# Kernel optimization log

Hardware: AMD Instinct MI355X
Metric: run time of the kernel (lower is better)

Reference implementation:

```python
import jax, jax.numpy as jnp
import numpy as np

E = 400000   # total edges
G = 64       # num graphs
H = 256      # hidden_dim
NN = 20000   # node id range
FRONTIER_BONUS = 0.5


def layer_norm(x, g, b, eps=1e-5):
    m = jnp.mean(x, axis=-1, keepdims=True)
    v = jnp.var(x, axis=-1, keepdims=True)
    return (x - m) / jnp.sqrt(v + eps) * g + b


def setup_inputs() -> dict:
    key = jax.random.key(0)
    ks = jax.random.split(key, 20)
    s = 0.02
    inp = {
        "edge_tokens": jax.random.normal(ks[0], (E, H), jnp.float32),
        "question_tokens": jax.random.normal(ks[1], (G, H), jnp.float32),
        "edge_batch": jnp.sort(jax.random.randint(ks[2], (E,), 0, G)),
        "selected_mask": jax.random.bernoulli(ks[3], 0.3, (E,)),
        "edge_heads": jax.random.randint(ks[4], (E,), 0, NN),
        "edge_tails": jax.random.randint(ks[5], (E,), 0, NN),
        "current_tail": jax.random.randint(ks[6], (G,), 0, NN),
        # edge_proj params: LayerNorm(H+2) -> Linear(H+2,H) -> GELU -> Linear(H,H) -> GELU
        "ln1_g": jnp.ones((H + 2,), jnp.float32),
        "ln1_b": jnp.zeros((H + 2,), jnp.float32),
        "W1": s * jax.random.normal(ks[7], (H + 2, H), jnp.float32),
        "b1": jnp.zeros((H,), jnp.float32),
        "W2": s * jax.random.normal(ks[8], (H, H), jnp.float32),
        "b2": jnp.zeros((H,), jnp.float32),
        # selection_head: Linear(H,1)
        "sel_w": s * jax.random.normal(ks[9], (H, 1), jnp.float32),
        "sel_b": jnp.zeros((1,), jnp.float32),
        # stop_head: LayerNorm(2H) -> Linear(2H,H) -> GELU -> Linear(H,1)
        "ln2_g": jnp.ones((2 * H,), jnp.float32),
        "ln2_b": jnp.zeros((2 * H,), jnp.float32),
        "sW1": s * jax.random.normal(ks[10], (2 * H, H), jnp.float32),
        "sb1": jnp.zeros((H,), jnp.float32),
        "sW2": s * jax.random.normal(ks[11], (H, 1), jnp.float32),
        "sb2": jnp.zeros((1,), jnp.float32),
    }
    return inp


def reference(edge_tokens, question_tokens, edge_batch, selected_mask,
              edge_heads, edge_tails, current_tail,
              ln1_g, ln1_b, W1, b1, W2, b2, sel_w, sel_b,
              ln2_g, ln2_b, sW1, sb1, sW2, sb2):
    num_graphs = question_tokens.shape[0]
    candidate = ~selected_mask
    cur_e = current_tail[edge_batch]                       # [E] gather by graph id
    frontier = candidate & ((edge_heads == cur_e) | (edge_tails == cur_e))
    aux = jnp.stack([candidate.astype(jnp.float32), frontier.astype(jnp.float32)], axis=-1)
    x = jnp.concatenate([edge_tokens, aux], axis=-1)       # [E, H+2]
    h = layer_norm(x, ln1_g, ln1_b)
    h = jax.nn.gelu(h @ W1 + b1, approximate=False)        # Dropout is identity in eval
    h = jax.nn.gelu(h @ W2 + b2, approximate=False)        # edge_repr [E, H]
    edge_logits = (h @ sel_w)[:, 0] + sel_b[0]
    edge_logits = edge_logits + FRONTIER_BONUS * frontier.astype(jnp.float32)
    counts = jax.ops.segment_sum(jnp.ones((h.shape[0],), jnp.float32), edge_batch, num_segments=num_graphs)
    counts = jnp.clip(counts, 1.0)                          # bincount.clamp(min=1)
    pooled = jax.ops.segment_sum(h, edge_batch, num_segments=num_graphs) / counts[:, None]
    s_in = jnp.concatenate([pooled, question_tokens], axis=-1)  # [G, 2H]
    s = layer_norm(s_in, ln2_g, ln2_b)
    s = jax.nn.gelu(s @ sW1 + sb1, approximate=False)
    stop_logits = (s @ sW2)[:, 0] + sb2[0]
    return edge_logits, stop_logits, pooled
```

## Files before the change

### kernel.cpp

```cpp
#include <hip/hip_runtime.h>
#include <hip/hip_bf16.h>
#include <cstdint>


typedef __bf16 bf16x8 __attribute__((ext_vector_type(8)));
typedef float  f32x4  __attribute__((ext_vector_type(4)));

typedef __attribute__((address_space(1))) const char gas_char;
typedef __attribute__((address_space(3))) char las_char;

__device__ __forceinline__ float gelu_f(float x) {
  float x2 = x * x;
  float t1 = __builtin_fmaf(0.1029444f, x2, 2.3022078f);
  float a  = x * t1;
  float e;
  asm("v_exp_f32 %0, %1" : "=v"(e) : "v"(a));
  float r;
  asm("v_rcp_f32 %0, %1" : "=v"(r) : "v"(e + 1.0f));
  return x - x * r;
}

__global__ void prep_pack(const float* __restrict__ W1, const float* __restrict__ W2,
                          const float* __restrict__ ln1g,
                          __bf16* __restrict__ W1p, __bf16* __restrict__ W2p) {
  int gid = blockIdx.x * blockDim.x + threadIdx.x;
  int m  = gid >> 13;
  int b  = (gid >> 6) & 127;
  int l  = gid & 63;
  int kt = b >> 4, nt = b & 15;
  int k0 = kt * 32 + ((l >> 4) << 3);
  int n  = nt * 16 + (l & 15);
  const float* W = m ? W2 : W1;
  bf16x8 v;
#pragma unroll
  for (int i = 0; i < 8; ++i) {
    int k = k0 + i;
    float wv = W[k * 256 + n];
    if (!m) wv *= ln1g[k];
    v[i] = (__bf16)wv;
  }
  __bf16* dst = m ? W2p : W1p;
  *(bf16x8*)(dst + (size_t)(b * 64 + l) * 8) = v;
}

__global__ void prep_vec(const float* __restrict__ W1, const float* __restrict__ ln1g,
                         const float* __restrict__ ln1b, const float* __restrict__ b1,
                         const unsigned* __restrict__ smask_words,
                         float* __restrict__ C0, float* __restrict__ GW6,
                         float* __restrict__ GW7, int* __restrict__ maskIsByte) {
  __shared__ float red[4][256];
  const int n = threadIdx.x & 255, c = threadIdx.x >> 8;
  const int k0 = c * 64, k1 = (c == 3) ? 258 : k0 + 64;
  float s = 0.f;
#pragma unroll 4
  for (int k = k0; k < k1; ++k) s += ln1b[k] * W1[k * 256 + n];
  red[c][n] = s;
  __syncthreads();
  if (c == 0) {
    C0[n]  = b1[n] + red[0][n] + red[1][n] + red[2][n] + red[3][n];
    GW6[n] = ln1g[256] * W1[256 * 256 + n];
    GW7[n] = ln1g[257] * W1[257 * 256 + n];
  }
  if (threadIdx.x == 0) {
    int big = 0;
    for (int i = 0; i < 64; ++i) { if (smask_words[i] > 1u) big = 1; }
    *maskIsByte = big;
  }
}

#define EPB 64

__device__ __forceinline__ void stage4(const char* gsrc, char* ldst) {
  __builtin_amdgcn_global_load_lds((gas_char*)gsrc, (las_char*)ldst, 16, 0, 0);
  __builtin_amdgcn_global_load_lds((gas_char*)(gsrc + 1024), (las_char*)(ldst + 1024), 16, 0, 0);
  __builtin_amdgcn_global_load_lds((gas_char*)(gsrc + 2048), (las_char*)(ldst + 2048), 16, 0, 0);
  __builtin_amdgcn_global_load_lds((gas_char*)(gsrc + 3072), (las_char*)(ldst + 3072), 16, 0, 0);
}

__device__ __forceinline__ void gemm8(const char* __restrict__ Wp, const char* nextWp,
                                      char* B0, char* B1,
                                      const char* aBase, unsigned swA, unsigned gA,
                                      int bOff, int woff, int l16, f32x4 (&acc)[4][4]) {
#pragma unroll
  for (int kt = 0; kt < 8; ++kt) {
    if (kt == 0) asm volatile("s_waitcnt vmcnt(4)" ::: "memory");
    else         asm volatile("s_waitcnt vmcnt(0)" ::: "memory");
    __builtin_amdgcn_s_barrier();
    if (kt >= 1 && kt < 7)
      stage4(Wp + (kt + 1) * 16384 + woff + l16, ((kt & 1) ? B0 : B1) + woff);
    if (kt == 7 && nextWp)
      stage4(nextWp + woff + l16, B0 + woff);
    const char* bb = (kt & 1) ? B1 : B0;
    bf16x8 av[4], bv[4];
#pragma unroll
    for (int rf = 0; rf < 4; ++rf)
      av[rf] = *(const bf16x8*)(aBase + rf * 8192 + (((unsigned)(kt * 64) + gA) ^ swA));
#pragma unroll
    for (int cf = 0; cf < 4; ++cf)
      bv[cf] = *(const bf16x8*)(bb + bOff + (cf << 10));
#pragma unroll
    for (int rf = 0; rf < 4; ++rf)
#pragma unroll
      for (int cf = 0; cf < 4; ++cf)
        acc[rf][cf] = __builtin_amdgcn_mfma_f32_16x16x32_bf16(av[rf], bv[cf], acc[rf][cf], 0, 0, 0);
  }
  __builtin_amdgcn_s_barrier();
}

__global__ __launch_bounds__(256, 2) void edge_kernel(
    const float* __restrict__ tok, const int* __restrict__ ebatch,
    const unsigned char* __restrict__ smaskB,
    const int* __restrict__ eheads, const int* __restrict__ etails,
    const int* __restrict__ curtail,
    const __bf16* __restrict__ W1p, const __bf16* __restrict__ W2p,
    const float* __restrict__ C0v, const float* __restrict__ GW6v,
    const float* __restrict__ GW7v, const float* __restrict__ b2v,
    const float* __restrict__ selwv, const float* __restrict__ selbv,
    const int* __restrict__ maskFlag,
    float* __restrict__ outLogits, float* __restrict__ pooledAcc,
    float* __restrict__ cnts) {
  __shared__ __align__(16) char As_[64 * 512];
  __shared__ __align__(16) char Bs_[2][16384];
  __shared__ float sZa0[64], sZa1[64], sFront[64];
  __shared__ float sLog[64][4];
  __shared__ int sG[64];

  const int t = threadIdx.x;
  const int w = t >> 6, l = t & 63;
  const int base = blockIdx.x * EPB;
  const int l16 = l << 4;
  const int woff = __builtin_amdgcn_readfirstlane(w << 12);

  const char* W1c = (const char*)W1p;
  const char* W2c = (const char*)W2p;

  stage4(W1c + woff + l16, Bs_[0] + woff);
  stage4(W1c + 16384 + woff + l16, Bs_[1] + woff);

  if (t < 64) {
    int ge = base + t;
    int g  = ebatch[ge];
    int mb = *maskFlag;
    int mv = mb ? (int)smaskB[ge] : ((const int*)smaskB)[ge];
    int cand = (mv == 0);
    int cur  = curtail[g];
    int fr   = cand && ((eheads[ge] == cur) || (etails[ge] == cur));
    sZa0[t] = (float)cand; sZa1[t] = (float)fr; sFront[t] = (float)fr; sG[t] = g;
  }
  __syncthreads();

  if (t == 0) {
    int cg = sG[0]; float run = 1.f;
    for (int e = 1; e < EPB; ++e) {
      int g = sG[e];
      if (g == cg) run += 1.f;
      else { atomicAdd(&cnts[cg], run); cg = g; run = 1.f; }
    }
    atomicAdd(&cnts[cg], run);
  }

  {
    const int e = t >> 2, q = t & 3;
    const float* rp = tok + (size_t)(base + e) * 256 + q * 4;
    float4 v[16];
    float s = 0.f, s2 = 0.f;
#pragma unroll
    for (int j = 0; j < 16; ++j) {
      v[j] = *(const float4*)(rp + j * 16);
      s  += v[j].x + v[j].y + v[j].z + v[j].w;
      s2 += v[j].x * v[j].x + v[j].y * v[j].y + v[j].z * v[j].z + v[j].w * v[j].w;
    }
    float a0 = 0.f, a1 = 0.f;
    if (q == 0) { a0 = sZa0[e]; a1 = sZa1[e]; s += a0 + a1; s2 += a0 + a1; }
    s  += __shfl_xor(s, 1);  s  += __shfl_xor(s, 2);
    s2 += __shfl_xor(s2, 1); s2 += __shfl_xor(s2, 2);
    const float mean = s * (1.0f / 258.0f);
    const float var  = s2 * (1.0f / 258.0f) - mean * mean;
    const float rstd = rsqrtf(var + 1e-5f);
    const unsigned sw = (unsigned)(e & 7) << 4;
#pragma unroll
    for (int j = 0; j < 16; ++j) {
      union { __bf16 h[4]; uint2 u; } cv;
      cv.h[0] = (__bf16)((v[j].x - mean) * rstd);
      cv.h[1] = (__bf16)((v[j].y - mean) * rstd);
      cv.h[2] = (__bf16)((v[j].z - mean) * rstd);
      cv.h[3] = (__bf16)((v[j].w - mean) * rstd);
      unsigned off = (unsigned)(q * 8 + j * 32);
      *(uint2*)(As_ + e * 512 + (off ^ sw)) = cv.u;
    }
    if (q == 0) {
      sZa0[e] = (a0 - mean) * rstd;
      sZa1[e] = (a1 - mean) * rstd;
    }
  }
  __syncthreads();

  const int rA = l & 15;
  const int r0 = (l >> 4) << 2;
  float c0r[4], w6r[4], w7r[4], b2r[4], lwr[4];
  const float selbr = selbv[0];
#pragma unroll
  for (int cf = 0; cf < 4; ++cf) {
    int col = w * 64 + cf * 16 + rA;
    c0r[cf] = C0v[col]; w6r[cf] = GW6v[col]; w7r[cf] = GW7v[col];
    b2r[cf] = b2v[col]; lwr[cf] = selwv[col];
  }
  f32x4 za0q[4], za1q[4];
#pragma unroll
  for (int rf = 0; rf < 4; ++rf) {
    za0q[rf] = *(const f32x4*)&sZa0[rf * 16 + r0];
    za1q[rf] = *(const f32x4*)&sZa1[rf * 16 + r0];
  }
  f32x4 acc[4][4];
#pragma unroll
  for (int rf = 0; rf < 4; ++rf)
#pragma unroll
    for (int cf = 0; cf < 4; ++cf)
#pragma unroll
      for (int i = 0; i < 4; ++i)
        acc[rf][cf][i] = c0r[cf] + za0q[rf][i] * w6r[cf] + za1q[rf][i] * w7r[cf];

  const unsigned swA = (unsigned)(rA & 7) << 4;
  const unsigned gA  = (unsigned)((l >> 4) << 4);
  const char* aBase  = As_ + rA * 512;
  const int bOff     = (w << 12) + l16;

  gemm8(W1c, W2c, Bs_[0], Bs_[1], aBase, swA, gA, bOff, woff, l16, acc);

#pragma unroll
  for (int rf = 0; rf < 4; ++rf)
#pragma unroll
    for (int i = 0; i < 4; ++i) {
      int row = rf * 16 + r0 + i;
      char* rowp = As_ + row * 512;
      unsigned sw = (unsigned)(row & 7) << 4;
#pragma unroll
      for (int cf = 0; cf < 4; ++cf) {
        int col = w * 64 + cf * 16 + rA;
        *(__bf16*)(rowp + (((unsigned)(col * 2)) ^ sw)) = (__bf16)gelu_f(acc[rf][cf][i]);
      }
    }
  stage4(W2c + 16384 + woff + l16, Bs_[1] + woff);
  __syncthreads();

#pragma unroll
  for (int rf = 0; rf < 4; ++rf)
#pragma unroll
    for (int cf = 0; cf < 4; ++cf)
#pragma unroll
      for (int i = 0; i < 4; ++i) acc[rf][cf][i] = b2r[cf];
  gemm8(W2c, nullptr, Bs_[0], Bs_[1], aBase, swA, gA, bOff, woff, l16, acc);

#pragma unroll
  for (int rf = 0; rf < 4; ++rf)
#pragma unroll
    for (int cf = 0; cf < 4; ++cf)
#pragma unroll
      for (int i = 0; i < 4; ++i) acc[rf][cf][i] = gelu_f(acc[rf][cf][i]);

#pragma unroll
  for (int rf = 0; rf < 4; ++rf)
#pragma unroll
    for (int i = 0; i < 4; ++i) {
      float p = acc[rf][0][i] * lwr[0] + acc[rf][1][i] * lwr[1]
              + acc[rf][2][i] * lwr[2] + acc[rf][3][i] * lwr[3];
      p += __shfl_xor(p, 1); p += __shfl_xor(p, 2);
      p += __shfl_xor(p, 4); p += __shfl_xor(p, 8);
      if (rA == 0) sLog[rf * 16 + r0 + i][w] = p;
    }
  __syncthreads();
  if (t < 64)
    outLogits[base + t] = sLog[t][0] + sLog[t][1] + sLog[t][2] + sLog[t][3]
                        + selbr + 0.5f * sFront[t];

  if (sG[0] == sG[EPB - 1]) {
    int g = sG[0];
#pragma unroll
    for (int cf = 0; cf < 4; ++cf) {
      float sv = 0.f;
#pragma unroll
      for (int rf = 0; rf < 4; ++rf)
#pragma unroll
        for (int i = 0; i < 4; ++i) sv += acc[rf][cf][i];
      sv += __shfl_xor(sv, 16);
      sv += __shfl_xor(sv, 32);
      if (l < 16) atomicAdd(&pooledAcc[g * 256 + w * 64 + cf * 16 + l], sv);
    }
  } else {
#pragma unroll
    for (int rf = 0; rf < 4; ++rf)
#pragma unroll
      for (int i = 0; i < 4; ++i) {
        int row = rf * 16 + r0 + i;
        int g = sG[row];
#pragma unroll
        for (int cf = 0; cf < 4; ++cf)
          atomicAdd(&pooledAcc[g * 256 + w * 64 + cf * 16 + rA], acc[rf][cf][i]);
      }
  }
}

__global__ __launch_bounds__(256) void stop_kernel(
    const float* __restrict__ pooledAcc, const float* __restrict__ cnts,
    const float* __restrict__ qtok,
    const float* __restrict__ ln2g, const float* __restrict__ ln2b,
    const float* __restrict__ sW1, const float* __restrict__ sb1,
    const float* __restrict__ sW2, const float* __restrict__ sb2,
    float* __restrict__ outStop, float* __restrict__ outPooled) {
  __shared__ float sIn[512], sLn[512], sRed[8];
  const int t = threadIdx.x, g = blockIdx.x;
  const int w = t >> 6, l = t & 63;
  float c = fmaxf(cnts[g], 1.0f);
  float p = pooledAcc[g * 256 + t] / c;
  outPooled[g * 256 + t] = p;
  sIn[t] = p;
  sIn[256 + t] = qtok[g * 256 + t];
  __syncthreads();
  float a = sIn[t], b = sIn[256 + t];
  float s = a + b, s2 = a * a + b * b;
#pragma unroll
  for (int m = 1; m < 64; m <<= 1) { s += __shfl_xor(s, m); s2 += __shfl_xor(s2, m); }
  if (l == 0) { sRed[w] = s; sRed[4 + w] = s2; }
  __syncthreads();
  s  = sRed[0] + sRed[1] + sRed[2] + sRed[3];
  s2 = sRed[4] + sRed[5] + sRed[6] + sRed[7];
  const float mean = s * (1.0f / 512.0f);
  const float var  = s2 * (1.0f / 512.0f) - mean * mean;
  const float rstd = rsqrtf(var + 1e-5f);
  sLn[t]       = (a - mean) * rstd * ln2g[t] + ln2b[t];
  sLn[256 + t] = (b - mean) * rstd * ln2g[256 + t] + ln2b[256 + t];
  __syncthreads();
  float accv = sb1[t];
#pragma unroll 8
  for (int k = 0; k < 512; ++k) accv += sLn[k] * sW1[k * 256 + t];
  float u = gelu_f(accv);
  float part = u * sW2[t];
#pragma unroll
  for (int m = 1; m < 64; m <<= 1) part += __shfl_xor(part, m);
  if (l == 0) sRed[w] = part;
  __syncthreads();
  if (t == 0) outStop[g] = sRed[0] + sRed[1] + sRed[2] + sRed[3] + sb2[0];
}

extern "C" void kernel_launch(void* const* d_in, const int* in_sizes, int n_in,
                              void* d_out, int out_size, void* d_ws, size_t ws_size,
                              hipStream_t stream) {
  const float* tok   = (const float*)d_in[0];
  const float* qtok  = (const float*)d_in[1];
  const int* ebatch  = (const int*)d_in[2];
  const void* smask  = d_in[3];
  const int* eheads  = (const int*)d_in[4];
  const int* etails  = (const int*)d_in[5];
  const int* curtail = (const int*)d_in[6];
  const float* ln1g  = (const float*)d_in[7];
  const float* ln1b  = (const float*)d_in[8];
  const float* W1    = (const float*)d_in[9];
  const float* b1    = (const float*)d_in[10];
  const float* W2    = (const float*)d_in[11];
  const float* b2    = (const float*)d_in[12];
  const float* selw  = (const float*)d_in[13];
  const float* selb  = (const float*)d_in[14];
  const float* ln2g  = (const float*)d_in[15];
  const float* ln2b  = (const float*)d_in[16];
  const float* sW1   = (const float*)d_in[17];
  const float* sb1   = (const float*)d_in[18];
  const float* sW2   = (const float*)d_in[19];
  const float* sb2   = (const float*)d_in[20];

  const int E = in_sizes[2];
  const int G = in_sizes[1] / 256;

  char* ws = (char*)d_ws;
  __bf16* W1p   = (__bf16*)(ws);
  __bf16* W2p   = (__bf16*)(ws + 131072);
  float*  C0    = (float*)(ws + 262144);
  float*  GW6   = (float*)(ws + 263168);
  float*  GW7   = (float*)(ws + 264192);
  float*  pooled= (float*)(ws + 265216);
  float*  cnts  = (float*)(ws + 330752);
  int*    mflag = (int*)(ws + 331008);
  (void)ws_size; (void)n_in; (void)out_size;

  hipMemsetAsync(ws + 265216, 0, 65536 + 256, stream);

  prep_pack<<<64, 256, 0, stream>>>(W1, W2, ln1g, W1p, W2p);
  prep_vec<<<1, 1024, 0, stream>>>(W1, ln1g, ln1b, b1, (const unsigned*)smask,
                                   C0, GW6, GW7, mflag);
  edge_kernel<<<E / EPB, 256, 0, stream>>>(
      tok, ebatch, (const unsigned char*)smask, eheads, etails, curtail,
      W1p, W2p, C0, GW6, GW7, b2, selw, selb, mflag,
      (float*)d_out, pooled, cnts);
  stop_kernel<<<G, 256, 0, stream>>>(pooled, cnts, qtok, ln2g, ln2b,
                                     sW1, sb1, sW2, sb2,
                                     (float*)d_out + E, (float*)d_out + E + G);
}
```

Before: 350.6 us.

## Make edge kernel persistent with per-wave 32-edge tiles and LDS-resident W1

Replaces the one-block-per-64-edges kernel with a persistent grid of 256 blocks of 512 threads. W1 is loaded once into 128KB of LDS per block, and each wave independently processes 32-edge tiles. The layer norm and the first GEMM keep activations in registers as MFMA B operands, and the hidden layer is redistributed via shuffles, not an LDS round trip. W2 is streamed from global/L2 directly into registers with double buffering. This removes block barriers and repeated weight staging, but adds pressure on registers and on L2 bandwidth for W2, and the 128KB of LDS limits occupancy.

```diff
diff --git a/kernel.cpp b/kernel.cpp
--- a/kernel.cpp
+++ b/kernel.cpp
@@ -18,6 +18,14 @@
   float r;
   asm("v_rcp_f32 %0, %1" : "=v"(r) : "v"(e + 1.0f));
   return x - x * r;
+}
+
+__device__ __forceinline__ bf16x8 as_frag(uint4 u) {
+  union { uint4 u; bf16x8 f; } c; c.u = u; return c.f;
+}
+__device__ __forceinline__ unsigned pk2(float a, float b) {
+  union { __bf16 h[2]; unsigned u; } c;
+  c.h[0] = (__bf16)a; c.h[1] = (__bf16)b; return c.u;
 }
 
 __global__ void prep_pack(const float* __restrict__ W1, const float* __restrict__ W2,
@@ -68,46 +76,7 @@
   }
 }
 
-#define EPB 64
-
-__device__ __forceinline__ void stage4(const char* gsrc, char* ldst) {
-  __builtin_amdgcn_global_load_lds((gas_char*)gsrc, (las_char*)ldst, 16, 0, 0);
-  __builtin_amdgcn_global_load_lds((gas_char*)(gsrc + 1024), (las_char*)(ldst + 1024), 16, 0, 0);
-  __builtin_amdgcn_global_load_lds((gas_char*)(gsrc + 2048), (las_char*)(ldst + 2048), 16, 0, 0);
-  __builtin_amdgcn_global_load_lds((gas_char*)(gsrc + 3072), (las_char*)(ldst + 3072), 16, 0, 0);
-}
-
-__device__ __forceinline__ void gemm8(const char* __restrict__ Wp, const char* nextWp,
-                                      char* B0, char* B1,
-                                      const char* aBase, unsigned swA, unsigned gA,
-                                      int bOff, int woff, int l16, f32x4 (&acc)[4][4]) {
-#pragma unroll
-  for (int kt = 0; kt < 8; ++kt) {
-    if (kt == 0) asm volatile("s_waitcnt vmcnt(4)" ::: "memory");
-    else         asm volatile("s_waitcnt vmcnt(0)" ::: "memory");
-    __builtin_amdgcn_s_barrier();
-    if (kt >= 1 && kt < 7)
-      stage4(Wp + (kt + 1) * 16384 + woff + l16, ((kt & 1) ? B0 : B1) + woff);
-    if (kt == 7 && nextWp)
-      stage4(nextWp + woff + l16, B0 + woff);
-    const char* bb = (kt & 1) ? B1 : B0;
-    bf16x8 av[4], bv[4];
-#pragma unroll
-    for (int rf = 0; rf < 4; ++rf)
-      av[rf] = *(const bf16x8*)(aBase + rf * 8192 + (((unsigned)(kt * 64) + gA) ^ swA));
-#pragma unroll
-    for (int cf = 0; cf < 4; ++cf)
-      bv[cf] = *(const bf16x8*)(bb + bOff + (cf << 10));
-#pragma unroll
-    for (int rf = 0; rf < 4; ++rf)
-#pragma unroll
-      for (int cf = 0; cf < 4; ++cf)
-        acc[rf][cf] = __builtin_amdgcn_mfma_f32_16x16x32_bf16(av[rf], bv[cf], acc[rf][cf], 0, 0, 0);
-  }
-  __builtin_amdgcn_s_barrier();
-}
-
-__global__ __launch_bounds__(256, 2) void edge_kernel(
+__global__ __launch_bounds__(512, 2) void edge_kernel(
     const float* __restrict__ tok, const int* __restrict__ ebatch,
     const unsigned char* __restrict__ smaskB,
     const int* __restrict__ eheads, const int* __restrict__ etails,
@@ -118,184 +87,257 @@
     const float* __restrict__ selwv, const float* __restrict__ selbv,
     const int* __restrict__ maskFlag,
     float* __restrict__ outLogits, float* __restrict__ pooledAcc,
-    float* __restrict__ cnts) {
-  __shared__ __align__(16) char As_[64 * 512];
-  __shared__ __align__(16) char Bs_[2][16384];
-  __shared__ float sZa0[64], sZa1[64], sFront[64];
-  __shared__ float sLog[64][4];
-  __shared__ int sG[64];
-
-  const int t = threadIdx.x;
-  const int w = t >> 6, l = t & 63;
-  const int base = blockIdx.x * EPB;
-  const int l16 = l << 4;
-  const int woff = __builtin_amdgcn_readfirstlane(w << 12);
-
-  const char* W1c = (const char*)W1p;
+    float* __restrict__ cnts, int E) {
+  __shared__ __align__(16) char Wlds[131072];
+  __shared__ float sC0[256], sW6[256], sW7[256], sSelw[256], sB2[256];
+
+  const int t  = threadIdx.x;
+  const int w  = t >> 6, l = t & 63;
+  const int lo = l & 15, g = l >> 4;
+
+  {
+    const char* Wsrc = (const char*)W1p;
+    unsigned woff = __builtin_amdgcn_readfirstlane((unsigned)w * 16384u);
+#pragma unroll
+    for (int it = 0; it < 16; ++it)
+      __builtin_amdgcn_global_load_lds((gas_char*)(Wsrc + woff + it * 1024 + l * 16),
+                                       (las_char*)(Wlds + woff + it * 1024), 16, 0, 0);
+  }
+  if (t < 256) {
+    sC0[t] = C0v[t]; sW6[t] = GW6v[t]; sW7[t] = GW7v[t];
+    sSelw[t] = selwv[t]; sB2[t] = b2v[t];
+  }
+  const int   mb    = *maskFlag;
+  const float selbr = selbv[0];
+  __syncthreads();
+
+  const int totalTiles = E >> 5;
+  const int nWaves = gridDim.x * 8;
   const char* W2c = (const char*)W2p;
 
-  stage4(W1c + woff + l16, Bs_[0] + woff);
-  stage4(W1c + 16384 + woff + l16, Bs_[1] + woff);
-
-  if (t < 64) {
-    int ge = base + t;
-    int g  = ebatch[ge];
-    int mb = *maskFlag;
-    int mv = mb ? (int)smaskB[ge] : ((const int*)smaskB)[ge];
-    int cand = (mv == 0);
-    int cur  = curtail[g];
-    int fr   = cand && ((eheads[ge] == cur) || (etails[ge] == cur));
-    sZa0[t] = (float)cand; sZa1[t] = (float)fr; sFront[t] = (float)fr; sG[t] = g;
-  }
-  __syncthreads();
-
-  if (t == 0) {
-    int cg = sG[0]; float run = 1.f;
-    for (int e = 1; e < EPB; ++e) {
-      int g = sG[e];
-      if (g == cg) run += 1.f;
-      else { atomicAdd(&cnts[cg], run); cg = g; run = 1.f; }
+  for (int tile = blockIdx.x * 8 + w; tile < totalTiles; tile += nWaves) {
+    const int base = tile << 5;
+
+    float candf = 0.f, frontf = 0.f; int gid = 0;
+    if (l < 32) {
+      int ge = base + l;
+      gid = ebatch[ge];
+      int mv = mb ? (int)smaskB[ge] : ((const int*)smaskB)[ge];
+      int cand = (mv == 0);
+      int cur  = curtail[gid];
+      int fr   = cand && ((eheads[ge] == cur) || (etails[ge] == cur));
+      candf = (float)cand; frontf = (float)fr;
     }
-    atomicAdd(&cnts[cg], run);
-  }
-
-  {
-    const int e = t >> 2, q = t & 3;
-    const float* rp = tok + (size_t)(base + e) * 256 + q * 4;
-    float4 v[16];
-    float s = 0.f, s2 = 0.f;
-#pragma unroll
-    for (int j = 0; j < 16; ++j) {
-      v[j] = *(const float4*)(rp + j * 16);
-      s  += v[j].x + v[j].y + v[j].z + v[j].w;
-      s2 += v[j].x * v[j].x + v[j].y * v[j].y + v[j].z * v[j].z + v[j].w * v[j].w;
+    const int g0s = __shfl(gid, 0);
+    const bool uniform =
+        (__ballot((l < 32) ? (gid == g0s) : 1) == ~0ull);
+    {
+      int gp = __shfl(gid, (l == 0) ? 0 : l - 1);
+      bool isb = (l < 32) && (l == 0 || gid != gp);
+      unsigned long long bm = __ballot(isb);
+      if (isb) {
+        unsigned long long m2 = bm >> (l + 1);
+        int run = m2 ? (int)__ffsll((long long)m2) : (32 - l);
+        atomicAdd(&cnts[gid], (float)run);
+      }
     }
-    float a0 = 0.f, a1 = 0.f;
-    if (q == 0) { a0 = sZa0[e]; a1 = sZa1[e]; s += a0 + a1; s2 += a0 + a1; }
-    s  += __shfl_xor(s, 1);  s  += __shfl_xor(s, 2);
-    s2 += __shfl_xor(s2, 1); s2 += __shfl_xor(s2, 2);
-    const float mean = s * (1.0f / 258.0f);
-    const float var  = s2 * (1.0f / 258.0f) - mean * mean;
-    const float rstd = rsqrtf(var + 1e-5f);
-    const unsigned sw = (unsigned)(e & 7) << 4;
-#pragma unroll
-    for (int j = 0; j < 16; ++j) {
-      union { __bf16 h[4]; uint2 u; } cv;
-      cv.h[0] = (__bf16)((v[j].x - mean) * rstd);
-      cv.h[1] = (__bf16)((v[j].y - mean) * rstd);
-      cv.h[2] = (__bf16)((v[j].z - mean) * rstd);
-      cv.h[3] = (__bf16)((v[j].w - mean) * rstd);
-      unsigned off = (unsigned)(q * 8 + j * 32);
-      *(uint2*)(As_ + e * 512 + (off ^ sw)) = cv.u;
+    const float ca = __shfl(candf, lo),      fa = __shfl(frontf, lo);
+    const float cb = __shfl(candf, 16 + lo), fb = __shfl(frontf, 16 + lo);
+
+    uint4 zlnA[8], zlnB[8];
+    float za0a, za1a, za0b, za1b;
+#pragma unroll
+    for (int rr = 0; rr < 2; ++rr) {
+      const int   edge = base + rr * 16 + lo;
+      const float aux0 = rr ? cb : ca, aux1 = rr ? fb : fa;
+      const float* rp = tok + (size_t)edge * 256 + (g << 3);
+      float4 v[16];
+#pragma unroll
+      for (int kt = 0; kt < 8; ++kt) {
+        v[2 * kt]     = *(const float4*)(rp + kt * 32);
+        v[2 * kt + 1] = *(const float4*)(rp + kt * 32 + 4);
+      }
+      float s = 0.f, s2 = 0.f;
+#pragma unroll
+      for (int j = 0; j < 16; ++j) {
+        s  += v[j].x + v[j].y + v[j].z + v[j].w;
+        s2 += v[j].x * v[j].x + v[j].y * v[j].y + v[j].z * v[j].z + v[j].w * v[j].w;
+      }
+      s  += __shfl_xor(s, 16);  s  += __shfl_xor(s, 32);
+      s2 += __shfl_xor(s2, 16); s2 += __shfl_xor(s2, 32);
+      s += aux0 + aux1; s2 += aux0 + aux1;
+      const float mean = s * (1.0f / 258.0f);
+      const float var  = s2 * (1.0f / 258.0f) - mean * mean;
+      const float rstd = rsqrtf(var + 1e-5f);
+      const float nm   = -mean * rstd;
+      uint4* zf = rr ? zlnB : zlnA;
+#pragma unroll
+      for (int kt = 0; kt < 8; ++kt) {
+        union { __bf16 h[8]; uint4 u; } cv;
+#pragma unroll
+        for (int q = 0; q < 4; ++q) {
+          float x0 = (q < 2) ? ((q & 1) ? v[2*kt].z : v[2*kt].x)
+                             : ((q & 1) ? v[2*kt+1].z : v[2*kt+1].x);
+          float x1 = (q < 2) ? ((q & 1) ? v[2*kt].w : v[2*kt].y)
+                             : ((q & 1) ? v[2*kt+1].w : v[2*kt+1].y);
+          cv.h[2*q]   = (__bf16)__builtin_fmaf(x0, rstd, nm);
+          cv.h[2*q+1] = (__bf16)__builtin_fmaf(x1, rstd, nm);
+        }
+        zf[kt] = cv.u;
+      }
+      if (rr) { za0b = __builtin_fmaf(aux0, rstd, nm); za1b = __builtin_fmaf(aux1, rstd, nm); }
+      else    { za0a = __builtin_fmaf(aux0, rstd, nm); za1a = __builtin_fmaf(aux1, rstd, nm); }
     }
-    if (q == 0) {
-      sZa0[e] = (a0 - mean) * rstd;
-      sZa1[e] = (a1 - mean) * rstd;
+
+    uint4 h1f[2][8];
+#pragma unroll
+    for (int half = 0; half < 2; ++half) {
+      f32x4 acc[8][2];
+#pragma unroll
+      for (int jl = 0; jl < 8; ++jl) {
+        const int j = half * 8 + jl;
+        f32x4 c0 = *(const f32x4*)&sC0[j * 16 + g * 4];
+        f32x4 w6 = *(const f32x4*)&sW6[j * 16 + g * 4];
+        f32x4 w7 = *(const f32x4*)&sW7[j * 16 + g * 4];
+#pragma unroll
+        for (int i = 0; i < 4; ++i) {
+          acc[jl][0][i] = c0[i] + za0a * w6[i] + za1a * w7[i];
+          acc[jl][1][i] = c0[i] + za0b * w6[i] + za1b * w7[i];
+        }
+      }
+#pragma unroll
+      for (int kt = 0; kt < 8; ++kt) {
+        bf16x8 afr[8];
+#pragma unroll
+        for (int jl = 0; jl < 8; ++jl)
+          afr[jl] = as_frag(*(const uint4*)(Wlds + (size_t)(kt * 16 + half * 8 + jl) * 1024 + l * 16));
+        bf16x8 bA = as_frag(zlnA[kt]), bB = as_frag(zlnB[kt]);
+#pragma unroll
+        for (int jl = 0; jl < 8; ++jl) {
+          acc[jl][0] = __builtin_amdgcn_mfma_f32_16x16x32_bf16(afr[jl], bA, acc[jl][0], 0, 0, 0);
+          acc[jl][1] = __builtin_amdgcn_mfma_f32_16x16x32_bf16(afr[jl], bB, acc[jl][1], 0, 0, 0);
+        }
+      }
+      unsigned pk[2][8][2];
+#pragma unroll
+      for (int mt = 0; mt < 2; ++mt)
+#pragma unroll
+        for (int jl = 0; jl < 8; ++jl) {
+          pk[mt][jl][0] = pk2(gelu_f(acc[jl][mt][0]), gelu_f(acc[jl][mt][1]));
+          pk[mt][jl][1] = pk2(gelu_f(acc[jl][mt][2]), gelu_f(acc[jl][mt][3]));
+        }
+#pragma unroll
+      for (int mt = 0; mt < 2; ++mt)
+#pragma unroll
+        for (int k2l = 0; k2l < 4; ++k2l) {
+          unsigned dw[4];
+#pragma unroll
+          for (int tt = 0; tt < 4; ++tt) {
+            int src = 16 * (2 * (g & 1) + (tt >> 1)) + lo;
+            unsigned dE = __shfl(pk[mt][2 * k2l][tt & 1], src);
+            unsigned dO = __shfl(pk[mt][2 * k2l + 1][tt & 1], src);
+            dw[tt] = (g >= 2) ? dO : dE;
+          }
+          h1f[mt][half * 4 + k2l] = make_uint4(dw[0], dw[1], dw[2], dw[3]);
+        }
     }
-  }
-  __syncthreads();
-
-  const int rA = l & 15;
-  const int r0 = (l >> 4) << 2;
-  float c0r[4], w6r[4], w7r[4], b2r[4], lwr[4];
-  const float selbr = selbv[0];
-#pragma unroll
-  for (int cf = 0; cf < 4; ++cf) {
-    int col = w * 64 + cf * 16 + rA;
-    c0r[cf] = C0v[col]; w6r[cf] = GW6v[col]; w7r[cf] = GW7v[col];
-    b2r[cf] = b2v[col]; lwr[cf] = selwv[col];
-  }
-  f32x4 za0q[4], za1q[4];
-#pragma unroll
-  for (int rf = 0; rf < 4; ++rf) {
-    za0q[rf] = *(const f32x4*)&sZa0[rf * 16 + r0];
-    za1q[rf] = *(const f32x4*)&sZa1[rf * 16 + r0];
-  }
-  f32x4 acc[4][4];
-#pragma unroll
-  for (int rf = 0; rf < 4; ++rf)
-#pragma unroll
-    for (int cf = 0; cf < 4; ++cf)
-#pragma unroll
-      for (int i = 0; i < 4; ++i)
-        acc[rf][cf][i] = c0r[cf] + za0q[rf][i] * w6r[cf] + za1q[rf][i] * w7r[cf];
-
-  const unsigned swA = (unsigned)(rA & 7) << 4;
-  const unsigned gA  = (unsigned)((l >> 4) << 4);
-  const char* aBase  = As_ + rA * 512;
-  const int bOff     = (w << 12) + l16;
-
-  gemm8(W1c, W2c, Bs_[0], Bs_[1], aBase, swA, gA, bOff, woff, l16, acc);
-
-#pragma unroll
-  for (int rf = 0; rf < 4; ++rf)
-#pragma unroll
-    for (int i = 0; i < 4; ++i) {
-      int row = rf * 16 + r0 + i;
-      char* rowp = As_ + row * 512;
-      unsigned sw = (unsigned)(row & 7) << 4;
-#pragma unroll
-      for (int cf = 0; cf < 4; ++cf) {
-        int col = w * 64 + cf * 16 + rA;
-        *(__bf16*)(rowp + (((unsigned)(col * 2)) ^ sw)) = (__bf16)gelu_f(acc[rf][cf][i]);
+
+    float plog[2][4];
+#pragma unroll
+    for (int mt = 0; mt < 2; ++mt)
+#pragma unroll
+      for (int i = 0; i < 4; ++i) plog[mt][i] = 0.f;
+
+#pragma unroll
+    for (int ch = 0; ch < 2; ++ch) {
+      f32x4 acc2[8][2];
+#pragma unroll
+      for (int c8 = 0; c8 < 8; ++c8) {
+        float bb = sB2[(ch * 8 + c8) * 16 + lo];
+#pragma unroll
+        for (int mt = 0; mt < 2; ++mt)
+#pragma unroll
+          for (int i = 0; i < 4; ++i) acc2[c8][mt][i] = bb;
+      }
+      const char* wbase = W2c + (size_t)ch * 8192 + (size_t)l * 16;
+      uint4 b0[8], b1[8];
+#pragma unroll
+      for (int c8 = 0; c8 < 8; ++c8) b0[c8] = *(const uint4*)(wbase + c8 * 1024);
+#pragma unroll
+      for (int kt2 = 0; kt2 < 8; ++kt2) {
+        if (kt2 < 7) {
+          if (kt2 & 1) {
+#pragma unroll
+            for (int c8 = 0; c8 < 8; ++c8)
+              b0[c8] = *(const uint4*)(wbase + (size_t)(kt2 + 1) * 16384 + c8 * 1024);
+          } else {
+#pragma unroll
+            for (int c8 = 0; c8 < 8; ++c8)
+              b1[c8] = *(const uint4*)(wbase + (size_t)(kt2 + 1) * 16384 + c8 * 1024);
+          }
+        }
+        bf16x8 a0 = as_frag(h1f[0][kt2]), a1 = as_frag(h1f[1][kt2]);
+#pragma unroll
+        for (int c8 = 0; c8 < 8; ++c8) {
+          bf16x8 bf = as_frag((kt2 & 1) ? b1[c8] : b0[c8]);
+          acc2[c8][0] = __builtin_amdgcn_mfma_f32_16x16x32_bf16(a0, bf, acc2[c8][0], 0, 0, 0);
+          acc2[c8][1] = __builtin_amdgcn_mfma_f32_16x16x32_bf16(a1, bf, acc2[c8][1], 0, 0, 0);
+        }
+      }
+#pragma unroll
+      for (int c8 = 0; c8 < 8; ++c8) {
+        float wv = sSelw[(ch * 8 + c8) * 16 + lo];
+#pragma unroll
+        for (int mt = 0; mt < 2; ++mt)
+#pragma unroll
+          for (int i = 0; i < 4; ++i) {
+            acc2[c8][mt][i] = gelu_f(acc2[c8][mt][i]);
+            plog[mt][i] += acc2[c8][mt][i] * wv;
+          }
+      }
+      if (uniform) {
+#pragma unroll
+        for (int c8 = 0; c8 < 8; ++c8) {
+          float pv = 0.f;
+#pragma unroll
+          for (int mt = 0; mt < 2; ++mt)
+#pragma unroll
+            for (int i = 0; i < 4; ++i) pv += acc2[c8][mt][i];
+          pv += __shfl_xor(pv, 16);
+          pv += __shfl_xor(pv, 32);
+          if (l < 16) atomicAdd(&pooledAcc[g0s * 256 + (ch * 8 + c8) * 16 + l], pv);
+        }
+      } else {
+        int gm[2][4];
+#pragma unroll
+        for (int mt = 0; mt < 2; ++mt)
+#pragma unroll
+          for (int i = 0; i < 4; ++i) gm[mt][i] = __shfl(gid, 16 * mt + 4 * g + i);
+#pragma unroll
+        for (int c8 = 0; c8 < 8; ++c8)
+#pragma unroll
+          for (int mt = 0; mt < 2; ++mt)
+#pragma unroll
+            for (int i = 0; i < 4; ++i)
+              atomicAdd(&pooledAcc[gm[mt][i] * 256 + (ch * 8 + c8) * 16 + lo],
+                        acc2[c8][mt][i]);
       }
     }
-  stage4(W2c + 16384 + woff + l16, Bs_[1] + woff);
-  __syncthreads();
-
-#pragma unroll
-  for (int rf = 0; rf < 4; ++rf)
-#pragma unroll
-    for (int cf = 0; cf < 4; ++cf)
-#pragma unroll
-      for (int i = 0; i < 4; ++i) acc[rf][cf][i] = b2r[cf];
-  gemm8(W2c, nullptr, Bs_[0], Bs_[1], aBase, swA, gA, bOff, woff, l16, acc);
-
-#pragma unroll
-  for (int rf = 0; rf < 4; ++rf)
-#pragma unroll
-    for (int cf = 0; cf < 4; ++cf)
-#pragma unroll
-      for (int i = 0; i < 4; ++i) acc[rf][cf][i] = gelu_f(acc[rf][cf][i]);
-
-#pragma unroll
-  for (int rf = 0; rf < 4; ++rf)
-#pragma unroll
-    for (int i = 0; i < 4; ++i) {
-      float p = acc[rf][0][i] * lwr[0] + acc[rf][1][i] * lwr[1]
-              + acc[rf][2][i] * lwr[2] + acc[rf][3][i] * lwr[3];
-      p += __shfl_xor(p, 1); p += __shfl_xor(p, 2);
-      p += __shfl_xor(p, 4); p += __shfl_xor(p, 8);
-      if (rA == 0) sLog[rf * 16 + r0 + i][w] = p;
-    }
-  __syncthreads();
-  if (t < 64)
-    outLogits[base + t] = sLog[t][0] + sLog[t][1] + sLog[t][2] + sLog[t][3]
-                        + selbr + 0.5f * sFront[t];
-
-  if (sG[0] == sG[EPB - 1]) {
-    int g = sG[0];
-#pragma unroll
-    for (int cf = 0; cf < 4; ++cf) {
-      float sv = 0.f;
-#pragma unroll
-      for (int rf = 0; rf < 4; ++rf)
-#pragma unroll
-        for (int i = 0; i < 4; ++i) sv += acc[rf][cf][i];
-      sv += __shfl_xor(sv, 16);
-      sv += __shfl_xor(sv, 32);
-      if (l < 16) atomicAdd(&pooledAcc[g * 256 + w * 64 + cf * 16 + l], sv);
-    }
-  } else {
-#pragma unroll
-    for (int rf = 0; rf < 4; ++rf)
+
+    float fm[2][4];
+#pragma unroll
+    for (int mt = 0; mt < 2; ++mt)
+#pragma unroll
+      for (int i = 0; i < 4; ++i) fm[mt][i] = __shfl(frontf, 16 * mt + 4 * g + i);
+#pragma unroll
+    for (int mt = 0; mt < 2; ++mt)
 #pragma unroll
       for (int i = 0; i < 4; ++i) {
-        int row = rf * 16 + r0 + i;
-        int g = sG[row];
-#pragma unroll
-        for (int cf = 0; cf < 4; ++cf)
-          atomicAdd(&pooledAcc[g * 256 + w * 64 + cf * 16 + rA], acc[rf][cf][i]);
+        float p = plog[mt][i];
+        p += __shfl_xor(p, 1); p += __shfl_xor(p, 2);
+        p += __shfl_xor(p, 4); p += __shfl_xor(p, 8);
+        if (lo == 0)
+          outLogits[base + 16 * mt + 4 * g + i] = p + selbr + 0.5f * fm[mt][i];
       }
   }
 }
@@ -386,10 +428,10 @@
   prep_pack<<<64, 256, 0, stream>>>(W1, W2, ln1g, W1p, W2p);
   prep_vec<<<1, 1024, 0, stream>>>(W1, ln1g, ln1b, b1, (const unsigned*)smask,
                                    C0, GW6, GW7, mflag);
-  edge_kernel<<<E / EPB, 256, 0, stream>>>(
+  edge_kernel<<<256, 512, 0, stream>>>(
       tok, ebatch, (const unsigned char*)smask, eheads, etails, curtail,
       W1p, W2p, C0, GW6, GW7, b2, selw, selb, mflag,
-      (float*)d_out, pooled, cnts);
+      (float*)d_out, pooled, cnts, E);
   stop_kernel<<<G, 256, 0, stream>>>(pooled, cnts, qtok, ln2g, ln2b,
                                      sW1, sb1, sW2, sb2,
                                      (float*)d_out + E, (float*)d_out + E + G);
```

Measured after the change: 826.3 us. 136% more time.

## Load packed weight fragments directly into registers instead of staging through LDS

Applied to the files above, without the earlier changes.

Replaces the LDS double-buffered weight staging (global_load_lds plus barriers per k-tile) with per-wave direct global loads of B fragments into registers, prefetching the next k-tile while the current MFMAs run. This removes the 32KB weight LDS buffer and the per-k-tile barriers. It also drops the occupancy hint of two blocks per CU in the launch bounds and narrows the lifetime of several epilogue constants to ease register pressure. The trade-off is that every wave now reads weights from global/L2 on its own rather than sharing one staged copy, and global load latency sits closer to the MFMA chain.

```diff
diff --git a/kernel.cpp b/kernel.cpp
--- a/kernel.cpp
+++ b/kernel.cpp
@@ -5,9 +5,6 @@
 
 typedef __bf16 bf16x8 __attribute__((ext_vector_type(8)));
 typedef float  f32x4  __attribute__((ext_vector_type(4)));
-
-typedef __attribute__((address_space(1))) const char gas_char;
-typedef __attribute__((address_space(3))) char las_char;
 
 __device__ __forceinline__ float gelu_f(float x) {
   float x2 = x * x;
@@ -18,6 +15,10 @@
   float r;
   asm("v_rcp_f32 %0, %1" : "=v"(r) : "v"(e + 1.0f));
   return x - x * r;
+}
+
+__device__ __forceinline__ bf16x8 as_frag(uint4 u) {
+  union { uint4 u; bf16x8 f; } c; c.u = u; return c.f;
 }
 
 __global__ void prep_pack(const float* __restrict__ W1, const float* __restrict__ W2,
@@ -70,44 +71,37 @@
 
 #define EPB 64
 
-__device__ __forceinline__ void stage4(const char* gsrc, char* ldst) {
-  __builtin_amdgcn_global_load_lds((gas_char*)gsrc, (las_char*)ldst, 16, 0, 0);
-  __builtin_amdgcn_global_load_lds((gas_char*)(gsrc + 1024), (las_char*)(ldst + 1024), 16, 0, 0);
-  __builtin_amdgcn_global_load_lds((gas_char*)(gsrc + 2048), (las_char*)(ldst + 2048), 16, 0, 0);
-  __builtin_amdgcn_global_load_lds((gas_char*)(gsrc + 3072), (las_char*)(ldst + 3072), 16, 0, 0);
-}
-
-__device__ __forceinline__ void gemm8(const char* __restrict__ Wp, const char* nextWp,
-                                      char* B0, char* B1,
-                                      const char* aBase, unsigned swA, unsigned gA,
-                                      int bOff, int woff, int l16, f32x4 (&acc)[4][4]) {
+__device__ __forceinline__ void gemm8_reg(const char* __restrict__ Wp,
+                                          const char* aBase, unsigned swA,
+                                          unsigned gA, int bOff,
+                                          f32x4 (&acc)[4][4]) {
+  uint4 bv[4], bn[4];
+#pragma unroll
+  for (int cf = 0; cf < 4; ++cf)
+    bv[cf] = *(const uint4*)(Wp + bOff + (cf << 10));
 #pragma unroll
   for (int kt = 0; kt < 8; ++kt) {
-    if (kt == 0) asm volatile("s_waitcnt vmcnt(4)" ::: "memory");
-    else         asm volatile("s_waitcnt vmcnt(0)" ::: "memory");
-    __builtin_amdgcn_s_barrier();
-    if (kt >= 1 && kt < 7)
-      stage4(Wp + (kt + 1) * 16384 + woff + l16, ((kt & 1) ? B0 : B1) + woff);
-    if (kt == 7 && nextWp)
-      stage4(nextWp + woff + l16, B0 + woff);
-    const char* bb = (kt & 1) ? B1 : B0;
-    bf16x8 av[4], bv[4];
+    if (kt < 7) {
+#pragma unroll
+      for (int cf = 0; cf < 4; ++cf)
+        bn[cf] = *(const uint4*)(Wp + (kt + 1) * 16384 + bOff + (cf << 10));
+    }
+    bf16x8 av[4];
 #pragma unroll
     for (int rf = 0; rf < 4; ++rf)
       av[rf] = *(const bf16x8*)(aBase + rf * 8192 + (((unsigned)(kt * 64) + gA) ^ swA));
 #pragma unroll
-    for (int cf = 0; cf < 4; ++cf)
-      bv[cf] = *(const bf16x8*)(bb + bOff + (cf << 10));
-#pragma unroll
     for (int rf = 0; rf < 4; ++rf)
 #pragma unroll
       for (int cf = 0; cf < 4; ++cf)
-        acc[rf][cf] = __builtin_amdgcn_mfma_f32_16x16x32_bf16(av[rf], bv[cf], acc[rf][cf], 0, 0, 0);
-  }
-  __builtin_amdgcn_s_barrier();
-}
-
-__global__ __launch_bounds__(256, 2) void edge_kernel(
+        acc[rf][cf] = __builtin_amdgcn_mfma_f32_16x16x32_bf16(av[rf], as_frag(bv[cf]),
+                                                              acc[rf][cf], 0, 0, 0);
+#pragma unroll
+    for (int cf = 0; cf < 4; ++cf) bv[cf] = bn[cf];
+  }
+}
+
+__global__ __launch_bounds__(256) void edge_kernel(
     const float* __restrict__ tok, const int* __restrict__ ebatch,
     const unsigned char* __restrict__ smaskB,
     const int* __restrict__ eheads, const int* __restrict__ etails,
@@ -120,7 +114,6 @@
     float* __restrict__ outLogits, float* __restrict__ pooledAcc,
     float* __restrict__ cnts) {
   __shared__ __align__(16) char As_[64 * 512];
-  __shared__ __align__(16) char Bs_[2][16384];
   __shared__ float sZa0[64], sZa1[64], sFront[64];
   __shared__ float sLog[64][4];
   __shared__ int sG[64];
@@ -128,14 +121,6 @@
   const int t = threadIdx.x;
   const int w = t >> 6, l = t & 63;
   const int base = blockIdx.x * EPB;
-  const int l16 = l << 4;
-  const int woff = __builtin_amdgcn_readfirstlane(w << 12);
-
-  const char* W1c = (const char*)W1p;
-  const char* W2c = (const char*)W2p;
-
-  stage4(W1c + woff + l16, Bs_[0] + woff);
-  stage4(W1c + 16384 + woff + l16, Bs_[1] + woff);
 
   if (t < 64) {
     int ge = base + t;
@@ -197,35 +182,36 @@
 
   const int rA = l & 15;
   const int r0 = (l >> 4) << 2;
-  float c0r[4], w6r[4], w7r[4], b2r[4], lwr[4];
-  const float selbr = selbv[0];
-#pragma unroll
-  for (int cf = 0; cf < 4; ++cf) {
-    int col = w * 64 + cf * 16 + rA;
-    c0r[cf] = C0v[col]; w6r[cf] = GW6v[col]; w7r[cf] = GW7v[col];
-    b2r[cf] = b2v[col]; lwr[cf] = selwv[col];
-  }
-  f32x4 za0q[4], za1q[4];
-#pragma unroll
-  for (int rf = 0; rf < 4; ++rf) {
-    za0q[rf] = *(const f32x4*)&sZa0[rf * 16 + r0];
-    za1q[rf] = *(const f32x4*)&sZa1[rf * 16 + r0];
-  }
   f32x4 acc[4][4];
-#pragma unroll
-  for (int rf = 0; rf < 4; ++rf)
-#pragma unroll
-    for (int cf = 0; cf < 4; ++cf)
-#pragma unroll
-      for (int i = 0; i < 4; ++i)
-        acc[rf][cf][i] = c0r[cf] + za0q[rf][i] * w6r[cf] + za1q[rf][i] * w7r[cf];
+  {
+    float c0r[4], w6r[4], w7r[4];
+#pragma unroll
+    for (int cf = 0; cf < 4; ++cf) {
+      int col = w * 64 + cf * 16 + rA;
+      c0r[cf] = C0v[col]; w6r[cf] = GW6v[col]; w7r[cf] = GW7v[col];
+    }
+    f32x4 za0q[4], za1q[4];
+#pragma unroll
+    for (int rf = 0; rf < 4; ++rf) {
+      za0q[rf] = *(const f32x4*)&sZa0[rf * 16 + r0];
+      za1q[rf] = *(const f32x4*)&sZa1[rf * 16 + r0];
+    }
+#pragma unroll
+    for (int rf = 0; rf < 4; ++rf)
+#pragma unroll
+      for (int cf = 0; cf < 4; ++cf)
+#pragma unroll
+        for (int i = 0; i < 4; ++i)
+          acc[rf][cf][i] = c0r[cf] + za0q[rf][i] * w6r[cf] + za1q[rf][i] * w7r[cf];
+  }
 
   const unsigned swA = (unsigned)(rA & 7) << 4;
   const unsigned gA  = (unsigned)((l >> 4) << 4);
   const char* aBase  = As_ + rA * 512;
-  const int bOff     = (w << 12) + l16;
-
-  gemm8(W1c, W2c, Bs_[0], Bs_[1], aBase, swA, gA, bOff, woff, l16, acc);
+  const int bOff     = (w << 12) + (l << 4);
+
+  gemm8_reg((const char*)W1p, aBase, swA, gA, bOff, acc);
+  __syncthreads();
 
 #pragma unroll
   for (int rf = 0; rf < 4; ++rf)
@@ -240,38 +226,44 @@
         *(__bf16*)(rowp + (((unsigned)(col * 2)) ^ sw)) = (__bf16)gelu_f(acc[rf][cf][i]);
       }
     }
-  stage4(W2c + 16384 + woff + l16, Bs_[1] + woff);
-  __syncthreads();
+  __syncthreads();
+
+#pragma unroll
+  for (int cf = 0; cf < 4; ++cf) {
+    float bb = b2v[w * 64 + cf * 16 + rA];
+#pragma unroll
+    for (int rf = 0; rf < 4; ++rf)
+#pragma unroll
+      for (int i = 0; i < 4; ++i) acc[rf][cf][i] = bb;
+  }
+  gemm8_reg((const char*)W2p, aBase, swA, gA, bOff, acc);
 
 #pragma unroll
   for (int rf = 0; rf < 4; ++rf)
 #pragma unroll
     for (int cf = 0; cf < 4; ++cf)
 #pragma unroll
-      for (int i = 0; i < 4; ++i) acc[rf][cf][i] = b2r[cf];
-  gemm8(W2c, nullptr, Bs_[0], Bs_[1], aBase, swA, gA, bOff, woff, l16, acc);
-
-#pragma unroll
-  for (int rf = 0; rf < 4; ++rf)
-#pragma unroll
-    for (int cf = 0; cf < 4; ++cf)
-#pragma unroll
       for (int i = 0; i < 4; ++i) acc[rf][cf][i] = gelu_f(acc[rf][cf][i]);
 
-#pragma unroll
-  for (int rf = 0; rf < 4; ++rf)
-#pragma unroll
-    for (int i = 0; i < 4; ++i) {
-      float p = acc[rf][0][i] * lwr[0] + acc[rf][1][i] * lwr[1]
-              + acc[rf][2][i] * lwr[2] + acc[rf][3][i] * lwr[3];
-      p += __shfl_xor(p, 1); p += __shfl_xor(p, 2);
-      p += __shfl_xor(p, 4); p += __shfl_xor(p, 8);
-      if (rA == 0) sLog[rf * 16 + r0 + i][w] = p;
-    }
+  {
+    float lwr[4];
+#pragma unroll
+    for (int cf = 0; cf < 4; ++cf) lwr[cf] = selwv[w * 64 + cf * 16 + rA];
+#pragma unroll
+    for (int rf = 0; rf < 4; ++rf)
+#pragma unroll
+      for (int i = 0; i < 4; ++i) {
+        float p = acc[rf][0][i] * lwr[0] + acc[rf][1][i] * lwr[1]
+                + acc[rf][2][i] * lwr[2] + acc[rf][3][i] * lwr[3];
+        p += __shfl_xor(p, 1); p += __shfl_xor(p, 2);
+        p += __shfl_xor(p, 4); p += __shfl_xor(p, 8);
+        if (rA == 0) sLog[rf * 16 + r0 + i][w] = p;
+      }
+  }
   __syncthreads();
   if (t < 64)
     outLogits[base + t] = sLog[t][0] + sLog[t][1] + sLog[t][2] + sLog[t][3]
-                        + selbr + 0.5f * sFront[t];
+                        + selbv[0] + 0.5f * sFront[t];
 
   if (sG[0] == sG[EPB - 1]) {
     int g = sG[0];
```

After: 318.6 us. 9.1% less time.
